# Kernel optimization log

Measured on AMD Instinct MI355X. Metric: run time of the kernel, lower is better.

## Reference

```python
import jax, jax.numpy as jnp
import numpy as np

B, N, F, H = 2, 2048, 1024, 16
D = F // H  # head_dim = 64
SCALE = D ** -0.5


def setup_inputs() -> dict:
    key = jax.random.key(0)
    ks = jax.random.split(key, 5)
    std = F ** -0.5
    return {
        "x": jax.random.normal(ks[0], (B, N, F), dtype=jnp.float32),
        "Wq": jax.random.normal(ks[1], (F, F), dtype=jnp.float32) * std,
        "Wk": jax.random.normal(ks[2], (F, F), dtype=jnp.float32) * std,
        "Wv": jax.random.normal(ks[3], (F, F), dtype=jnp.float32) * std,
        "Wo": jax.random.normal(ks[4], (F, F), dtype=jnp.float32) * std,
        "bo": jnp.zeros((F,), dtype=jnp.float32),
    }


def reference(x, Wq, Wk, Wv, Wo, bo):
    b, n, f = x.shape
    # nn.Linear computes x @ W.T
    q = (x @ Wq.T).reshape(b, n, H, D).transpose(0, 2, 1, 3)  # bhnd
    k = (x @ Wk.T).reshape(b, n, H, D).transpose(0, 2, 1, 3)
    v = (x @ Wv.T).reshape(b, n, H, D).transpose(0, 2, 1, 3)
    score = jax.nn.softmax(jnp.einsum('bhif,bhjf->bhij', q, k) * SCALE, axis=-1)
    attn = jnp.einsum('bhij,bhjf->bihf', score, v)  # (b, n, h, d)
    o = attn.reshape(b, n, f) @ Wo.T + bo
    return o
```

## Files before the change

kernel.cpp:

```cpp
#include <hip/hip_runtime.h>
#include <hip/hip_bf16.h>

#define B_    2
#define NSEQ  2048
#define FDIM  1024
#define NH    16
#define HD    64
#define MTOT  (B_*NSEQ)
#define BHSZ  (NSEQ*HD)

typedef __bf16 bf16_t;
typedef __bf16 bf16x4 __attribute__((ext_vector_type(4)));
typedef __bf16 bf16x8 __attribute__((ext_vector_type(8)));
typedef float  f32x4  __attribute__((ext_vector_type(4)));

#define AS1 __attribute__((address_space(1)))
#define AS3 __attribute__((address_space(3)))

__device__ __forceinline__ void gld_lds16(const bf16_t* g, bf16_t* l) {
  __builtin_amdgcn_global_load_lds((const AS1 void*)g, (AS3 void*)l, 16, 0, 0);
}

__device__ __forceinline__ f32x4 mfma_pv(bf16x4 a, bf16x4 b, f32x4 c) {
#if defined(__HIP_DEVICE_COMPILE__)
#if __has_builtin(__builtin_amdgcn_mfma_f32_16x16x16bf16_1k)
  typedef short s4 __attribute__((ext_vector_type(4)));
  return __builtin_amdgcn_mfma_f32_16x16x16bf16_1k(
      __builtin_bit_cast(s4, a), __builtin_bit_cast(s4, b), c, 0, 0, 0);
#else
  asm("v_mfma_f32_16x16x16_bf16 %0, %1, %2, %0" : "+v"(c) : "v"(a), "v"(b));
  return c;
#endif
#else
  (void)a; (void)b;
  return c;
#endif
}

extern "C" __global__ __launch_bounds__(256) void cast_all_k(
    const float* __restrict__ x,  const float* __restrict__ wq,
    const float* __restrict__ wk, const float* __restrict__ wv,
    const float* __restrict__ wo,
    bf16_t* __restrict__ xb,  bf16_t* __restrict__ wqb,
    bf16_t* __restrict__ wkb, bf16_t* __restrict__ wvb,
    bf16_t* __restrict__ wob)
{
  long t = (long)blockIdx.x * blockDim.x + threadIdx.x;
  long i = t * 4;
  const float* src; bf16_t* dst; long off;
  if      (i < 4194304L) { src = x;  dst = xb;  off = i; }
  else if (i < 5242880L) { src = wq; dst = wqb; off = i - 4194304L; }
  else if (i < 6291456L) { src = wk; dst = wkb; off = i - 5242880L; }
  else if (i < 7340032L) { src = wv; dst = wvb; off = i - 6291456L; }
  else                   { src = wo; dst = wob; off = i - 7340032L; }
  float4 v = *(const float4*)(src + off);
  bf16x4 o = { (bf16_t)v.x, (bf16_t)v.y, (bf16_t)v.z, (bf16_t)v.w };
  *(bf16x4*)(dst + off) = o;
}

extern "C" __global__ __launch_bounds__(256) void gemm_bt_k(
    const bf16_t* __restrict__ A,
    const bf16_t* __restrict__ Bq, const bf16_t* __restrict__ Bk,
    const bf16_t* __restrict__ Bv,
    bf16_t* __restrict__ oq, bf16_t* __restrict__ okk,
    bf16_t* __restrict__ ovt, float* __restrict__ oo,
    const float* __restrict__ bias, int mode_base)
{
  __shared__ __align__(16) bf16_t As[128*32];
  __shared__ __align__(16) bf16_t Bs[128*32];
  const int K = FDIM;
  int mode = mode_base + blockIdx.z;
  const bf16_t* Bw = (mode == 0) ? Bq : (mode == 1) ? Bk : (mode == 2) ? Bv : Bq;
  int m0 = blockIdx.y * 128, n0 = blockIdx.x * 128;
  int tid = threadIdx.x, lane = tid & 63, wave = tid >> 6;
  int g = lane >> 4, c = lane & 15;
  int wm = (wave >> 1) * 64, wn = (wave & 1) * 64;
  f32x4 acc[4][4];
  for (int i = 0; i < 4; ++i)
    for (int j = 0; j < 4; ++j)
      acc[i][j] = (f32x4){0.f, 0.f, 0.f, 0.f};

  int srow = lane >> 2;
  int scol = (lane & 3) * 8;

  for (int kt = 0; kt < K / 32; ++kt) {
    int kk = kt * 32;
    for (int cc = 0; cc < 2; ++cc) {
      int chunk = wave * 2 + cc;
      const bf16_t* ag = A  + (long)(m0 + chunk*16 + srow) * K + kk + scol;
      const bf16_t* bg = Bw + (long)(n0 + chunk*16 + srow) * K + kk + scol;
      gld_lds16(ag, As + chunk * 512);
      gld_lds16(bg, Bs + chunk * 512);
    }
    __syncthreads();
    bf16x8 af[4], bfr[4];
    for (int t = 0; t < 4; ++t) {
      af[t]  = *(const bf16x8*)(As + (wm + t*16 + c) * 32 + g * 8);
      bfr[t] = *(const bf16x8*)(Bs + (wn + t*16 + c) * 32 + g * 8);
    }
    for (int mt = 0; mt < 4; ++mt)
      for (int nt = 0; nt < 4; ++nt)
        acc[mt][nt] = __builtin_amdgcn_mfma_f32_16x16x32_bf16(
            af[mt], bfr[nt], acc[mt][nt], 0, 0, 0);
    __syncthreads();
  }

  if (mode == 0) {
    for (int mt = 0; mt < 4; ++mt)
      for (int nt = 0; nt < 4; ++nt) {
        int n = n0 + wn + nt*16 + c;
        int h = n >> 6, d = n & 63;
        for (int r = 0; r < 4; ++r) {
          int m = m0 + wm + mt*16 + g*4 + r;
          int b = m >> 11, tok = m & 2047;
          oq[((long)(b*NH + h) * NSEQ + tok) * HD + d] =
              (bf16_t)(acc[mt][nt][r] * 0.125f);
        }
      }
  } else if (mode == 1) {
    for (int mt = 0; mt < 4; ++mt)
      for (int nt = 0; nt < 4; ++nt) {
        int n = n0 + wn + nt*16 + c;
        int h = n >> 6, d = n & 63;
        int kh = d >> 5, gK = (d >> 3) & 3, e = d & 7;
        for (int r = 0; r < 4; ++r) {
          int m = m0 + wm + mt*16 + g*4 + r;
          int b = m >> 11, tok = m & 2047;
          int tile = tok >> 6, mtA = (tok >> 4) & 3, cA = tok & 15;
          okk[(long)(b*NH + h) * BHSZ + tile*4096
              + (mtA*2 + kh)*512 + (gK*16 + cA)*8 + e] = (bf16_t)acc[mt][nt][r];
        }
      }
  } else if (mode == 2) {
    for (int mt = 0; mt < 4; ++mt)
      for (int nt = 0; nt < 4; ++nt) {
        int n = n0 + wn + nt*16 + c;
        int h = n >> 6, d = n & 63;
        int dtA = d >> 4, cA = d & 15;
        int m = m0 + wm + mt*16 + g*4;
        int b = m >> 11, tok = m & 2047;
        int tile = tok >> 6, mtA = (tok >> 4) & 3, gA = (tok >> 2) & 3;
        bf16x4 pk = { (bf16_t)acc[mt][nt][0], (bf16_t)acc[mt][nt][1],
                      (bf16_t)acc[mt][nt][2], (bf16_t)acc[mt][nt][3] };
        *(bf16x4*)(ovt + (long)(b*NH + h) * BHSZ + tile*4096
                   + (mtA*4 + dtA)*256 + (cA*4 + gA)*4) = pk;
      }
  } else {
    for (int mt = 0; mt < 4; ++mt)
      for (int nt = 0; nt < 4; ++nt) {
        int n = n0 + wn + nt*16 + c;
        float bv = bias[n];
        for (int r = 0; r < 4; ++r) {
          int m = m0 + wm + mt*16 + g*4 + r;
          oo[(long)m * FDIM + n] = acc[mt][nt][r] + bv;
        }
      }
  }
}

extern "C" __global__ __launch_bounds__(512) void attn_fused_k(
    const bf16_t* __restrict__ q, const bf16_t* __restrict__ k,
    const bf16_t* __restrict__ vt, bf16_t* __restrict__ attn)
{
  __shared__ __align__(16) char arena[65536];
  __shared__ float Ll[128];
  int bh = blockIdx.y;
  int tid = threadIdx.x, lane = tid & 63, wave = tid >> 6;
  int g = lane >> 4, c = lane & 15;
  int qg = wave & 3, half = wave >> 2;
  int qw = blockIdx.x * 128 + qg * 32;
  const bf16_t* Q  = q  + (long)bh * NSEQ * HD;
  const bf16_t* Kf = k  + (long)bh * BHSZ;
  const bf16_t* Vf = vt + (long)bh * BHSZ;

  bf16x8 bQ[2][2];
#pragma unroll
  for (int s = 0; s < 2; ++s)
#pragma unroll
    for (int hh = 0; hh < 2; ++hh)
      bQ[s][hh] = *(const bf16x8*)(Q + (long)(qw + s*16 + c) * HD + hh*32 + g*8);

  f32x4 acc[2][4];
  f32x4 lsum[2];
#pragma unroll
  for (int s = 0; s < 2; ++s) {
#pragma unroll
    for (int dt = 0; dt < 4; ++dt) acc[s][dt] = (f32x4){0.f, 0.f, 0.f, 0.f};
    lsum[s] = (f32x4){0.f, 0.f, 0.f, 0.f};
  }

  int w4 = wave & 3, ln = lane;
  const int NT = NSEQ / 128;
  int kbase = half * (NSEQ / 2);

  auto stage = [&](int buf, int k0) {
    bf16_t* Kb = (bf16_t*)(arena + buf * 32768 + half * 16384);
    bf16_t* Vb = Kb + 4096;
    long tbase = (long)(k0 >> 6) * 4096;
#pragma unroll
    for (int j = 0; j < 2; ++j) {
      int ch = j*4 + w4;
      gld_lds16(Kf + tbase + ch*512 + ln*8, Kb + ch*512);
      gld_lds16(Vf + tbase + ch*512 + ln*8, Vb + ch*512);
    }
  };

  stage(0, kbase);
  __syncthreads();

  for (int kt = 0; kt < NT; ++kt) {
    int cur = kt & 1;
    if (kt + 1 < NT) stage(cur ^ 1, kbase + (kt + 1) * 64);

    const bf16_t* Kb = (const bf16_t*)(arena + cur * 32768 + half * 16384);
    const bf16_t* Vb = Kb + 4096;

    f32x4 St[2][4];
#pragma unroll
    for (int mt = 0; mt < 4; ++mt) {
      bf16x8 k0f = *(const bf16x8*)(Kb + (mt*2 + 0) * 512 + lane * 8);
      bf16x8 k1f = *(const bf16x8*)(Kb + (mt*2 + 1) * 512 + lane * 8);
#pragma unroll
      for (int s = 0; s < 2; ++s) {
        f32x4 z = (f32x4){0.f, 0.f, 0.f, 0.f};
        z = __builtin_amdgcn_mfma_f32_16x16x32_bf16(k0f, bQ[s][0], z, 0, 0, 0);
        z = __builtin_amdgcn_mfma_f32_16x16x32_bf16(k1f, bQ[s][1], z, 0, 0, 0);
        St[s][mt] = z;
      }
    }

    bf16x4 bP[2][4];
#pragma unroll
    for (int s = 0; s < 2; ++s) {
#pragma unroll
      for (int mt = 0; mt < 4; ++mt) {
#pragma unroll
        for (int r = 0; r < 4; ++r) {
          float p = __expf(St[s][mt][r]);
          St[s][mt][r] = p;
          lsum[s][r] += p;
        }
        bP[s][mt] = (bf16x4){(bf16_t)St[s][mt][0], (bf16_t)St[s][mt][1],
                             (bf16_t)St[s][mt][2], (bf16_t)St[s][mt][3]};
      }
    }

#pragma unroll
    for (int mt = 0; mt < 4; ++mt)
#pragma unroll
      for (int dt = 0; dt < 4; ++dt) {
        bf16x4 aV = *(const bf16x4*)(Vb + (mt*4 + dt) * 256 + (c*4 + g) * 4);
        acc[0][dt] = mfma_pv(aV, bP[0][mt], acc[0][dt]);
        acc[1][dt] = mfma_pv(aV, bP[1][mt], acc[1][dt]);
      }

    __syncthreads();
  }

  float lp[2];
#pragma unroll
  for (int s = 0; s < 2; ++s) {
    float p = (lsum[s][0] + lsum[s][1]) + (lsum[s][2] + lsum[s][3]);
    p += __shfl_xor(p, 16);
    p += __shfl_xor(p, 32);
    lp[s] = p;
  }

  float* Opart = (float*)arena;
  bf16_t* Tb = (bf16_t*)(arena + 36864);
  if (half == 1) {
#pragma unroll
    for (int s = 0; s < 2; ++s) {
      int qrow = qg*32 + s*16 + c;
#pragma unroll
      for (int dt = 0; dt < 4; ++dt)
        *(f32x4*)(Opart + qrow*72 + dt*16 + g*4) = acc[s][dt];
      if (g == 0) Ll[qrow] = lp[s];
    }
  }
  __syncthreads();
  if (half == 0) {
#pragma unroll
    for (int s = 0; s < 2; ++s) {
      int qrow = qg*32 + s*16 + c;
      float inv = 1.f / (lp[s] + Ll[qrow]);
#pragma unroll
      for (int dt = 0; dt < 4; ++dt) {
        f32x4 part = *(const f32x4*)(Opart + qrow*72 + dt*16 + g*4);
#pragma unroll
        for (int r = 0; r < 4; ++r)
          Tb[qrow*80 + dt*16 + g*4 + r] =
              (bf16_t)((acc[s][dt][r] + part[r]) * inv);
      }
    }
  }
  __syncthreads();
  int b = bh >> 4, h = bh & 15;
  int row = tid >> 2, dseg = (tid & 3) * 16;
  const bf16_t* src = Tb + row*80 + dseg;
  bf16_t* dst = attn + ((long)(b * NSEQ + blockIdx.x*128 + row)) * FDIM + h * HD + dseg;
  *(bf16x8*)(dst)     = *(const bf16x8*)(src);
  *(bf16x8*)(dst + 8) = *(const bf16x8*)(src + 8);
}

extern "C" void kernel_launch(void* const* d_in, const int* in_sizes, int n_in,
                              void* d_out, int out_size, void* d_ws, size_t ws_size,
                              hipStream_t stream)
{
  const float* x  = (const float*)d_in[0];
  const float* wq = (const float*)d_in[1];
  const float* wk = (const float*)d_in[2];
  const float* wv = (const float*)d_in[3];
  const float* wo = (const float*)d_in[4];
  const float* bo = (const float*)d_in[5];
  float* out = (float*)d_out;
  char* ws = (char*)d_ws;

  const size_t MB = 1024 * 1024;
  bf16_t* xb    = (bf16_t*)(ws);
  bf16_t* wqb   = (bf16_t*)(ws + 8  * MB);
  bf16_t* wkb   = (bf16_t*)(ws + 10 * MB);
  bf16_t* wvb   = (bf16_t*)(ws + 12 * MB);
  bf16_t* wob   = (bf16_t*)(ws + 14 * MB);
  bf16_t* q_ws  = (bf16_t*)(ws + 16 * MB);
  bf16_t* k_ws  = (bf16_t*)(ws + 24 * MB);
  bf16_t* vt_ws = (bf16_t*)(ws + 32 * MB);
  bf16_t* at_ws = (bf16_t*)(ws + 40 * MB);

  hipLaunchKernelGGL(cast_all_k, dim3(8192), dim3(256), 0, stream,
                     x, wq, wk, wv, wo, xb, wqb, wkb, wvb, wob);

  hipLaunchKernelGGL(gemm_bt_k, dim3(8, 32, 3), dim3(256), 0, stream,
                     xb, wqb, wkb, wvb, q_ws, k_ws, vt_ws,
                     (float*)nullptr, (const float*)nullptr, 0);

  hipLaunchKernelGGL(attn_fused_k, dim3(16, 32), dim3(512), 0, stream,
                     q_ws, k_ws, vt_ws, at_ws);

  hipLaunchKernelGGL(gemm_bt_k, dim3(8, 32, 1), dim3(256), 0, stream,
                     at_ws, wob, wob, wob,
                     (bf16_t*)nullptr, (bf16_t*)nullptr, (bf16_t*)nullptr,
                     out, bo, 3);
}
```

Baseline: 203.7 us.

## Load K/V fragments straight to registers, drop LDS staging, use exp2

The attention kernel no longer stages K and V tiles through double-buffered LDS with per-iteration barriers. Each wave now reads its K and V MFMA fragments directly from global memory into registers, with the loop unrolled by two. The softmax exponent becomes a hardware exp2, with log2(e) folded into the Q scaling in the projection GEMM epilogue. This removes the in-loop __syncthreads and LDS round trips, but the four query-group waves now each fetch the same K/V tiles, leaning on L1/L2 and adding register pressure.

```diff
diff --git a/kernel.cpp b/kernel.cpp
--- a/kernel.cpp
+++ b/kernel.cpp
@@ -34,6 +34,18 @@
 #else
   (void)a; (void)b;
   return c;
+#endif
+}
+
+__device__ __forceinline__ float fexp2(float x) {
+#if defined(__HIP_DEVICE_COMPILE__)
+#if __has_builtin(__builtin_amdgcn_exp2f)
+  return __builtin_amdgcn_exp2f(x);
+#else
+  return exp2f(x);
+#endif
+#else
+  return exp2f(x);
 #endif
 }
 
@@ -106,6 +118,7 @@
   }
 
   if (mode == 0) {
+    const float QSC = 0.125f * 1.44269504088896340736f;
     for (int mt = 0; mt < 4; ++mt)
       for (int nt = 0; nt < 4; ++nt) {
         int n = n0 + wn + nt*16 + c;
@@ -114,7 +127,7 @@
           int m = m0 + wm + mt*16 + g*4 + r;
           int b = m >> 11, tok = m & 2047;
           oq[((long)(b*NH + h) * NSEQ + tok) * HD + d] =
-              (bf16_t)(acc[mt][nt][r] * 0.125f);
+              (bf16_t)(acc[mt][nt][r] * QSC);
         }
       }
   } else if (mode == 1) {
@@ -162,7 +175,8 @@
     const bf16_t* __restrict__ q, const bf16_t* __restrict__ k,
     const bf16_t* __restrict__ vt, bf16_t* __restrict__ attn)
 {
-  __shared__ __align__(16) char arena[65536];
+  __shared__ __align__(16) float Opart[128 * 68];
+  __shared__ __align__(16) bf16_t Tb[128 * 80];
   __shared__ float Ll[128];
   int bh = blockIdx.y;
   int tid = threadIdx.x, lane = tid & 63, wave = tid >> 6;
@@ -189,72 +203,58 @@
     lsum[s] = (f32x4){0.f, 0.f, 0.f, 0.f};
   }
 
-  int w4 = wave & 3, ln = lane;
   const int NT = NSEQ / 128;
-  int kbase = half * (NSEQ / 2);
-
-  auto stage = [&](int buf, int k0) {
-    bf16_t* Kb = (bf16_t*)(arena + buf * 32768 + half * 16384);
-    bf16_t* Vb = Kb + 4096;
-    long tbase = (long)(k0 >> 6) * 4096;
-#pragma unroll
-    for (int j = 0; j < 2; ++j) {
-      int ch = j*4 + w4;
-      gld_lds16(Kf + tbase + ch*512 + ln*8, Kb + ch*512);
-      gld_lds16(Vf + tbase + ch*512 + ln*8, Vb + ch*512);
-    }
-  };
-
-  stage(0, kbase);
-  __syncthreads();
-
+  int t0 = half * (NT);
+  int vslot = (c*4 + g) * 4;
+
+#pragma unroll 2
   for (int kt = 0; kt < NT; ++kt) {
-    int cur = kt & 1;
-    if (kt + 1 < NT) stage(cur ^ 1, kbase + (kt + 1) * 64);
-
-    const bf16_t* Kb = (const bf16_t*)(arena + cur * 32768 + half * 16384);
-    const bf16_t* Vb = Kb + 4096;
+    const bf16_t* tb = Kf + (long)(t0 + kt) * 4096;
+    const bf16_t* vb = Vf + (long)(t0 + kt) * 4096;
+
+    bf16x8 kf[4][2];
+#pragma unroll
+    for (int f = 0; f < 8; ++f)
+      kf[f >> 1][f & 1] = *(const bf16x8*)(tb + f*512 + lane*8);
+
+    bf16x4 vf[4][4];
+#pragma unroll
+    for (int fr = 0; fr < 16; ++fr)
+      vf[fr >> 2][fr & 3] = *(const bf16x4*)(vb + fr*256 + vslot);
 
     f32x4 St[2][4];
 #pragma unroll
-    for (int mt = 0; mt < 4; ++mt) {
-      bf16x8 k0f = *(const bf16x8*)(Kb + (mt*2 + 0) * 512 + lane * 8);
-      bf16x8 k1f = *(const bf16x8*)(Kb + (mt*2 + 1) * 512 + lane * 8);
+    for (int mt = 0; mt < 4; ++mt)
 #pragma unroll
       for (int s = 0; s < 2; ++s) {
         f32x4 z = (f32x4){0.f, 0.f, 0.f, 0.f};
-        z = __builtin_amdgcn_mfma_f32_16x16x32_bf16(k0f, bQ[s][0], z, 0, 0, 0);
-        z = __builtin_amdgcn_mfma_f32_16x16x32_bf16(k1f, bQ[s][1], z, 0, 0, 0);
+        z = __builtin_amdgcn_mfma_f32_16x16x32_bf16(kf[mt][0], bQ[s][0], z, 0, 0, 0);
+        z = __builtin_amdgcn_mfma_f32_16x16x32_bf16(kf[mt][1], bQ[s][1], z, 0, 0, 0);
         St[s][mt] = z;
       }
-    }
 
     bf16x4 bP[2][4];
 #pragma unroll
-    for (int s = 0; s < 2; ++s) {
+    for (int s = 0; s < 2; ++s)
 #pragma unroll
       for (int mt = 0; mt < 4; ++mt) {
 #pragma unroll
         for (int r = 0; r < 4; ++r) {
-          float p = __expf(St[s][mt][r]);
+          float p = fexp2(St[s][mt][r]);
           St[s][mt][r] = p;
           lsum[s][r] += p;
         }
         bP[s][mt] = (bf16x4){(bf16_t)St[s][mt][0], (bf16_t)St[s][mt][1],
                              (bf16_t)St[s][mt][2], (bf16_t)St[s][mt][3]};
       }
-    }
 
 #pragma unroll
     for (int mt = 0; mt < 4; ++mt)
 #pragma unroll
       for (int dt = 0; dt < 4; ++dt) {
-        bf16x4 aV = *(const bf16x4*)(Vb + (mt*4 + dt) * 256 + (c*4 + g) * 4);
-        acc[0][dt] = mfma_pv(aV, bP[0][mt], acc[0][dt]);
-        acc[1][dt] = mfma_pv(aV, bP[1][mt], acc[1][dt]);
-      }
-
-    __syncthreads();
+        acc[0][dt] = mfma_pv(vf[mt][dt], bP[0][mt], acc[0][dt]);
+        acc[1][dt] = mfma_pv(vf[mt][dt], bP[1][mt], acc[1][dt]);
+      }
   }
 
   float lp[2];
@@ -266,15 +266,13 @@
     lp[s] = p;
   }
 
-  float* Opart = (float*)arena;
-  bf16_t* Tb = (bf16_t*)(arena + 36864);
   if (half == 1) {
 #pragma unroll
     for (int s = 0; s < 2; ++s) {
       int qrow = qg*32 + s*16 + c;
 #pragma unroll
       for (int dt = 0; dt < 4; ++dt)
-        *(f32x4*)(Opart + qrow*72 + dt*16 + g*4) = acc[s][dt];
+        *(f32x4*)(Opart + qrow*68 + dt*16 + g*4) = acc[s][dt];
       if (g == 0) Ll[qrow] = lp[s];
     }
   }
@@ -286,7 +284,7 @@
       float inv = 1.f / (lp[s] + Ll[qrow]);
 #pragma unroll
       for (int dt = 0; dt < 4; ++dt) {
-        f32x4 part = *(const f32x4*)(Opart + qrow*72 + dt*16 + g*4);
+        f32x4 part = *(const f32x4*)(Opart + qrow*68 + dt*16 + g*4);
 #pragma unroll
         for (int r = 0; r < 4; ++r)
           Tb[qrow*80 + dt*16 + g*4 + r] =
```

New measurement: 291.1 us. +42.9%, slower.

## Double GEMM K-step to 64 and fold log2e into Q scale for exp2

Applied to the files above, without the earlier changes.

The projection GEMM now loads two 32-wide K slices per iteration into doubled LDS buffers, which halves the number of loop iterations and barrier pairs. Separately, the Q output scale absorbs log2(e), so the attention kernel can use the hardware exp2 instruction directly instead of __expf. The trade-off is more LDS per block, which may reduce occupancy, and the GEMM still has no overlap between loads and compute.

```diff
diff --git a/kernel.cpp b/kernel.cpp
--- a/kernel.cpp
+++ b/kernel.cpp
@@ -34,6 +34,18 @@
 #else
   (void)a; (void)b;
   return c;
+#endif
+}
+
+__device__ __forceinline__ float fexp2(float x) {
+#if defined(__HIP_DEVICE_COMPILE__)
+#if __has_builtin(__builtin_amdgcn_exp2f)
+  return __builtin_amdgcn_exp2f(x);
+#else
+  return exp2f(x);
+#endif
+#else
+  return exp2f(x);
 #endif
 }
 
@@ -66,8 +78,8 @@
     bf16_t* __restrict__ ovt, float* __restrict__ oo,
     const float* __restrict__ bias, int mode_base)
 {
-  __shared__ __align__(16) bf16_t As[128*32];
-  __shared__ __align__(16) bf16_t Bs[128*32];
+  __shared__ __align__(16) bf16_t As[2*128*32];
+  __shared__ __align__(16) bf16_t Bs[2*128*32];
   const int K = FDIM;
   int mode = mode_base + blockIdx.z;
   const bf16_t* Bw = (mode == 0) ? Bq : (mode == 1) ? Bk : (mode == 2) ? Bv : Bq;
@@ -83,29 +95,37 @@
   int srow = lane >> 2;
   int scol = (lane & 3) * 8;
 
-  for (int kt = 0; kt < K / 32; ++kt) {
-    int kk = kt * 32;
+  for (int kt = 0; kt < K / 64; ++kt) {
+    int kk = kt * 64;
     for (int cc = 0; cc < 2; ++cc) {
       int chunk = wave * 2 + cc;
       const bf16_t* ag = A  + (long)(m0 + chunk*16 + srow) * K + kk + scol;
       const bf16_t* bg = Bw + (long)(n0 + chunk*16 + srow) * K + kk + scol;
-      gld_lds16(ag, As + chunk * 512);
-      gld_lds16(bg, Bs + chunk * 512);
+      gld_lds16(ag,      As + chunk * 512);
+      gld_lds16(ag + 32, As + 4096 + chunk * 512);
+      gld_lds16(bg,      Bs + chunk * 512);
+      gld_lds16(bg + 32, Bs + 4096 + chunk * 512);
     }
     __syncthreads();
-    bf16x8 af[4], bfr[4];
+    bf16x8 af[4][2], bfr[4][2];
     for (int t = 0; t < 4; ++t) {
-      af[t]  = *(const bf16x8*)(As + (wm + t*16 + c) * 32 + g * 8);
-      bfr[t] = *(const bf16x8*)(Bs + (wn + t*16 + c) * 32 + g * 8);
-    }
-    for (int mt = 0; mt < 4; ++mt)
-      for (int nt = 0; nt < 4; ++nt)
+      af[t][0]  = *(const bf16x8*)(As + (wm + t*16 + c) * 32 + g * 8);
+      af[t][1]  = *(const bf16x8*)(As + 4096 + (wm + t*16 + c) * 32 + g * 8);
+      bfr[t][0] = *(const bf16x8*)(Bs + (wn + t*16 + c) * 32 + g * 8);
+      bfr[t][1] = *(const bf16x8*)(Bs + 4096 + (wn + t*16 + c) * 32 + g * 8);
+    }
+    for (int mt = 0; mt < 4; ++mt)
+      for (int nt = 0; nt < 4; ++nt) {
         acc[mt][nt] = __builtin_amdgcn_mfma_f32_16x16x32_bf16(
-            af[mt], bfr[nt], acc[mt][nt], 0, 0, 0);
+            af[mt][0], bfr[nt][0], acc[mt][nt], 0, 0, 0);
+        acc[mt][nt] = __builtin_amdgcn_mfma_f32_16x16x32_bf16(
+            af[mt][1], bfr[nt][1], acc[mt][nt], 0, 0, 0);
+      }
     __syncthreads();
   }
 
   if (mode == 0) {
+    const float QSC = 0.125f * 1.44269504088896340736f;
     for (int mt = 0; mt < 4; ++mt)
       for (int nt = 0; nt < 4; ++nt) {
         int n = n0 + wn + nt*16 + c;
@@ -114,7 +134,7 @@
           int m = m0 + wm + mt*16 + g*4 + r;
           int b = m >> 11, tok = m & 2047;
           oq[((long)(b*NH + h) * NSEQ + tok) * HD + d] =
-              (bf16_t)(acc[mt][nt][r] * 0.125f);
+              (bf16_t)(acc[mt][nt][r] * QSC);
         }
       }
   } else if (mode == 1) {
@@ -231,19 +251,18 @@
 
     bf16x4 bP[2][4];
 #pragma unroll
-    for (int s = 0; s < 2; ++s) {
+    for (int s = 0; s < 2; ++s)
 #pragma unroll
       for (int mt = 0; mt < 4; ++mt) {
 #pragma unroll
         for (int r = 0; r < 4; ++r) {
-          float p = __expf(St[s][mt][r]);
+          float p = fexp2(St[s][mt][r]);
           St[s][mt][r] = p;
           lsum[s][r] += p;
         }
         bP[s][mt] = (bf16x4){(bf16_t)St[s][mt][0], (bf16_t)St[s][mt][1],
                              (bf16_t)St[s][mt][2], (bf16_t)St[s][mt][3]};
       }
-    }
 
 #pragma unroll
     for (int mt = 0; mt < 4; ++mt)
```

Measured after the change: 203.9 us. No clear change (+0.1%).
